# Kernel optimization log

Measured on AMD Instinct MI355X. Metric: run time of the kernel, lower is better.

## Reference

```python
import math
import jax, jax.numpy as jnp
import numpy as np

B, T, C, H = 4, 2048, 1024, 16
HS = C // H


def setup_inputs() -> dict:
    key = jax.random.key(0)
    ks = jax.random.split(key, 5)
    s_in = 1.0 / math.sqrt(C)
    return {
        "x": jax.random.normal(ks[0], (B, T, C), dtype=jnp.float32),
        "w_attn": jax.random.normal(ks[1], (C, 3 * C), dtype=jnp.float32) * s_in,
        "b_attn": jax.random.normal(ks[2], (3 * C,), dtype=jnp.float32) * 0.02,
        "w_proj": jax.random.normal(ks[3], (C, C), dtype=jnp.float32) * s_in,
        "b_proj": jax.random.normal(ks[4], (C,), dtype=jnp.float32) * 0.02,
    }


def reference(x, w_attn, b_attn, w_proj, b_proj):
    Bx, Tx, Cx = x.shape
    hs = Cx // H
    qkv = x @ w_attn + b_attn  # [B, T, 3C]
    q, k, v = jnp.split(qkv, 3, axis=-1)
    # [B, H, T, hs]
    q = q.reshape(Bx, Tx, H, hs).transpose(0, 2, 1, 3)
    k = k.reshape(Bx, Tx, H, hs).transpose(0, 2, 1, 3)
    v = v.reshape(Bx, Tx, H, hs).transpose(0, 2, 1, 3)
    scale = 1.0 / math.sqrt(hs)
    att = jnp.einsum("bhqd,bhkd->bhqk", q, k) * scale  # [B, H, T, T]
    causal = jnp.tril(jnp.ones((Tx, Tx), dtype=bool))
    att = jnp.where(causal, att, -jnp.inf)
    att = jax.nn.softmax(att, axis=-1)
    y = jnp.einsum("bhqk,bhkd->bhqd", att, v)  # [B, H, T, hs]
    y = y.transpose(0, 2, 1, 3).reshape(Bx, Tx, Cx)
    return y @ w_proj + b_proj
```

## Files before the change

### kernel.cpp

```cpp
#include <hip/hip_runtime.h>
#include <stdint.h>

#define Bn 4
#define Tn 2048
#define Cn 1024
#define Hn 16
#define HSn 64
#define Mn (Bn*Tn)
#define N1n (3*Cn)

typedef unsigned short u16;
typedef unsigned int u32;
typedef __attribute__((ext_vector_type(8))) short short8;
typedef __attribute__((ext_vector_type(4))) float f32x4;
typedef __attribute__((ext_vector_type(16))) float f32x16;

__device__ __forceinline__ u16 f2bf(float f){
  u32 u = __float_as_uint(f);
  u += 0x7fffu + ((u >> 16) & 1u);
  return (u16)(u >> 16);
}

__device__ __forceinline__ u32 pkbf(float lo, float hi_){
  u32 r; asm("v_cvt_pk_bf16_f32 %0, %1, %2" : "=v"(r) : "v"(lo), "v"(hi_)); return r;
}

__device__ __forceinline__ float fexp2(float x){
  float r; asm("v_exp_f32 %0, %1" : "=v"(r) : "v"(x)); return r;
}

__device__ __forceinline__ void plswap(u32 &a, u32 &b){
  auto r = __builtin_amdgcn_permlane32_swap(a, b, false, false);
  a = r[0]; b = r[1];
}

__device__ __forceinline__ void gload_lds16(const void* g, void* l){
  __builtin_amdgcn_global_load_lds(
      (const __attribute__((address_space(1))) u32*)g,
      (__attribute__((address_space(3))) u32*)l, 16, 0, 0);
}

#define BARRIER() __builtin_amdgcn_s_barrier()
#define CFENCE() asm volatile("" ::: "memory")

__global__ void k_cvt(const float* __restrict__ in, u16* __restrict__ out, int n8){
  int i = blockIdx.x*256 + threadIdx.x;
  if (i >= n8) return;
  const float4* p = (const float4*)(in) + (size_t)i*2;
  float4 a = p[0], b = p[1];
  uint4 r;
  r.x = (u32)f2bf(a.x) | ((u32)f2bf(a.y) << 16);
  r.y = (u32)f2bf(a.z) | ((u32)f2bf(a.w) << 16);
  r.z = (u32)f2bf(b.x) | ((u32)f2bf(b.y) << 16);
  r.w = (u32)f2bf(b.z) | ((u32)f2bf(b.w) << 16);
  *((uint4*)(out) + i) = r;
}

__global__ void k_tcvt(const float* __restrict__ in, u16* __restrict__ out, int R, int Cc){
  __shared__ float sh[64][68];
  int tid = threadIdx.x;
  int c0 = blockIdx.x*64, r0 = blockIdx.y*64;
  int rr = tid >> 4, c4 = (tid & 15) * 4;
  #pragma unroll
  for (int p=0;p<4;p++){
    int r = rr + 16*p;
    *(float4*)&sh[r][c4] = *(const float4*)&in[(size_t)(r0+r)*Cc + c0 + c4];
  }
  __syncthreads();
  #pragma unroll
  for (int p=0;p<4;p++){
    int oc = rr + 16*p;
    u32 w0 = (u32)f2bf(sh[c4+0][oc]) | ((u32)f2bf(sh[c4+1][oc]) << 16);
    u32 w1 = (u32)f2bf(sh[c4+2][oc]) | ((u32)f2bf(sh[c4+3][oc]) << 16);
    uint2 pk; pk.x = w0; pk.y = w1;
    *(uint2*)&out[(size_t)(c0+oc)*R + r0 + c4] = pk;
  }
}

template <int MODE>
__global__ __launch_bounds__(256, 2)
void k_gemm2(const u16* __restrict__ A, const u16* __restrict__ Bt,
             const float* __restrict__ bias, void* __restrict__ Cout,
             u16* __restrict__ vt, int Nn_, int byPerXcd)
{
  extern __shared__ char smem[];
  const int nkt = 16;
  int tid = threadIdx.x;
  int wave = tid >> 6, lane = tid & 63, g = lane >> 4, cl = lane & 15;
  int wm = wave >> 1, wn = wave & 1;

  int xcd = blockIdx.x & 7, idx = blockIdx.x >> 3;
  int by = xcd * byPerXcd + (idx % byPerXcd);
  int bx = idx / byPerXcd;
  int m0 = by * 128, n0 = bx * 128;

  int srow = tid >> 3;
  int scolb = (tid & 7) << 4;
  int ssw = scolb ^ ((srow & 7) << 4);
  const char* Agp = (const char*)A  + (size_t)(m0 + srow) * 2048 + ssw;
  const char* Bgp = (const char*)Bt + (size_t)(n0 + srow) * 2048 + ssw;

  #define STG(t_, b_) { \
    const char* ag = Agp + (size_t)(t_)*128; \
    const char* bg = Bgp + (size_t)(t_)*128; \
    char* ab = smem + (b_)*32768 + (wave<<10); \
    char* bb = ab + 16384; \
    gload_lds16(ag,          ab); \
    gload_lds16(ag+ 65536,   ab+4096); \
    gload_lds16(ag+131072,   ab+8192); \
    gload_lds16(ag+196608,   ab+12288); \
    gload_lds16(bg,          bb); \
    gload_lds16(bg+ 65536,   bb+4096); \
    gload_lds16(bg+131072,   bb+8192); \
    gload_lds16(bg+196608,   bb+12288); }

  f32x4 acc[4][4];
  #pragma unroll
  for (int i=0;i<4;i++)
    #pragma unroll
    for (int j=0;j<4;j++) acc[i][j] = (f32x4){0.f,0.f,0.f,0.f};

  STG(0, 0);

  for (int t=0; t<nkt; ++t){
    int b = t & 1;
    if (t+1 < nkt){
      STG(t+1, b^1);
      asm volatile("s_waitcnt vmcnt(8)" ::: "memory");
    } else {
      asm volatile("s_waitcnt vmcnt(0)" ::: "memory");
    }
    BARRIER(); CFENCE();
    const char* Asb = smem + b*32768;
    const char* Bsb = Asb + 16384;
    short8 a[4][2], bq[4][2];
    #pragma unroll
    for (int i=0;i<4;i++){
      int row = wm*64 + i*16 + cl;
      #pragma unroll
      for (int ks=0;ks<2;ks++)
        a[i][ks] = *(const short8*)(Asb + row*128 + ((ks*64 + g*16) ^ ((row&7)<<4)));
    }
    #pragma unroll
    for (int j=0;j<4;j++){
      int row = wn*64 + j*16 + cl;
      #pragma unroll
      for (int ks=0;ks<2;ks++)
        bq[j][ks] = *(const short8*)(Bsb + row*128 + ((ks*64 + g*16) ^ ((row&7)<<4)));
    }
    asm volatile("s_waitcnt lgkmcnt(0)" ::: "memory");
    __builtin_amdgcn_s_setprio(1);
    #pragma unroll
    for (int ks=0;ks<2;ks++)
      #pragma unroll
      for (int i=0;i<4;i++)
        #pragma unroll
        for (int j=0;j<4;j++)
          acc[i][j] = __builtin_amdgcn_mfma_f32_16x16x32_bf16(a[i][ks], bq[j][ks], acc[i][j], 0, 0, 0);
    __builtin_amdgcn_s_setprio(0);
    CFENCE(); BARRIER(); CFENCE();
  }
  #undef STG

  #pragma unroll
  for (int jj=0;jj<4;jj++){
    int col = n0 + wn*64 + jj*16 + cl;
    float bj = bias[col];
    if (MODE == 0){
      #pragma unroll
      for (int i=0;i<4;i++){
        int rowb = m0 + wm*64 + i*16 + g*4;
        #pragma unroll
        for (int r=0;r<4;r++)
          ((float*)Cout)[(size_t)(rowb+r)*Nn_ + col] = acc[i][jj][r] + bj;
      }
    } else if (col < 2*Cn){
      #pragma unroll
      for (int i=0;i<4;i++){
        int rowb = m0 + wm*64 + i*16 + g*4;
        #pragma unroll
        for (int r=0;r<4;r++)
          ((u16*)Cout)[(size_t)(rowb+r)*Nn_ + col] = f2bf(acc[i][jj][r] + bj);
      }
    } else {
      int hd = col - 2*Cn;
      #pragma unroll
      for (int i=0;i<4;i++){
        int rowb = m0 + wm*64 + i*16 + g*4;
        int bb = rowb >> 11, tt = rowb & 2047;
        u16* dst = vt + (((size_t)(bb*16 + (hd>>6)))*64 + (hd&63))*2048 + tt;
        uint2 pk;
        pk.x = (u32)f2bf(acc[i][jj][0]+bj) | ((u32)f2bf(acc[i][jj][1]+bj) << 16);
        pk.y = (u32)f2bf(acc[i][jj][2]+bj) | ((u32)f2bf(acc[i][jj][3]+bj) << 16);
        *(uint2*)dst = pk;
      }
    }
  }
}

__global__ __launch_bounds__(256, 4)
void k_attn(const u16* __restrict__ qkv, const u16* __restrict__ vt, u16* __restrict__ yb){
  __shared__ __align__(16) u16 Ks[2][64*64];
  __shared__ __align__(16) u16 Vs[2][64*64];
  int tid = threadIdx.x, wave = tid >> 6, lane = tid & 63;
  int ql = lane & 31, hi = lane >> 5;
  int blk = blockIdx.x;
  int xcd = blk & 7, rest = blk >> 3;
  int bh  = xcd + 8*(rest & 7);
  int qt  = 15 - (rest >> 3);
  int b = bh >> 4, h = bh & 15;

  const u16* Kbase = qkv + (size_t)b*Tn*N1n + Cn + h*HSn;
  const u16* Vbase = vt  + (size_t)bh*HSn*Tn;

  auto STAGE = [&](int bufi, int kt){
    int kb_ = kt*64;
    #pragma unroll
    for (int it=0; it<2; ++it){
      int off = it*4096 + tid*16;
      int row = off >> 7;
      int cb  = off & 127;
      int gc  = (cb ^ ((row & 7) << 4)) >> 1;
      gload_lds16(Kbase + (size_t)(kb_ + row)*N1n + gc,
                  (char*)&Ks[bufi][0] + it*4096 + (wave << 10));
      gload_lds16(Vbase + (size_t)row*Tn + kb_ + gc,
                  (char*)&Vs[bufi][0] + it*4096 + (wave << 10));
    }
  };

  const float QSC = 0.125f * 1.44269504f;

  int q0 = qt * 128;
  int qw0 = q0 + wave*32;
  int qg  = qw0 + ql;
  int ntiles = 2*qt + 2;

  const u16* Qp = qkv + (size_t)(b*Tn + qg)*N1n + h*HSn;
  short8 qf[4];
  #pragma unroll
  for (int dc=0; dc<4; ++dc){
    union { short8 v; u32 w[4]; } qa;
    qa.v = *(const short8*)&Qp[dc*16 + hi*8];
    #pragma unroll
    for (int t=0; t<4; ++t){
      u32 w = qa.w[t];
      float lo = __uint_as_float(w << 16);
      float hf = __uint_as_float(w & 0xffff0000u);
      qa.w[t] = pkbf(lo*QSC, hf*QSC);
    }
    qf[dc] = qa.v;
  }

  f32x16 accO[2];
  #pragma unroll
  for (int f=0; f<2; ++f)
    #pragma unroll
    for (int r=0; r<16; ++r) accO[f][r] = 0.f;
  float m_ = -1e30f, l_ = 0.f;

  STAGE(0, 0);
  asm volatile("s_waitcnt vmcnt(0)" ::: "memory");
  __syncthreads();
  int buf = 0;

  for (int kt=0; kt<ntiles; ++kt){
    if (kt+1 < ntiles) STAGE(buf^1, kt+1);
    const char* Ksb = (const char*)&Ks[buf][0];
    const char* Vsb = (const char*)&Vs[buf][0];
    #pragma unroll
    for (int ksub=0; ksub<2; ++ksub){
      int kbase = kt*64 + ksub*32;
      if (kbase <= qw0 + 31){
        f32x16 s;
        #pragma unroll
        for (int r=0; r<16; ++r) s[r] = 0.f;
        __builtin_amdgcn_s_setprio(1);
        #pragma unroll
        for (int dc=0; dc<4; ++dc){
          short8 kf = *(const short8*)(Ksb + ((ksub*32 + ql) << 7)
                          + ((dc*32 + hi*16) ^ ((ql & 7) << 4)));
          s = __builtin_amdgcn_mfma_f32_32x32x16_bf16(kf, qf[dc], s, 0, 0, 0);
        }
        __builtin_amdgcn_s_setprio(0);
        float p[16];
        if (kbase + 31 > qw0){
          #pragma unroll
          for (int r=0; r<16; ++r){
            int krow = kbase + (r&3) + 8*(r>>2) + 4*hi;
            p[r] = (krow > qg) ? -1e30f : s[r];
          }
        } else {
          #pragma unroll
          for (int r=0; r<16; ++r) p[r] = s[r];
        }
        float t0 = fmaxf(fmaxf(fmaxf(p[0],p[1]),fmaxf(p[2],p[3])),
                         fmaxf(fmaxf(p[4],p[5]),fmaxf(p[6],p[7])));
        float t1 = fmaxf(fmaxf(fmaxf(p[8],p[9]),fmaxf(p[10],p[11])),
                         fmaxf(fmaxf(p[12],p[13]),fmaxf(p[14],p[15])));
        float tm = fmaxf(t0, t1);
        { u32 ua = __float_as_uint(tm), ub = ua; plswap(ua, ub);
          tm = fmaxf(__uint_as_float(ua), __uint_as_float(ub)); }
        if (!__all(tm - m_ <= 8.0f)){
          float mn = fmaxf(m_, tm);
          float al = fexp2(m_ - mn);
          m_ = mn; l_ *= al;
          #pragma unroll
          for (int f=0; f<2; ++f)
            #pragma unroll
            for (int r=0; r<16; ++r) accO[f][r] *= al;
        }
        float ls = 0.f;
        #pragma unroll
        for (int r=0; r<16; ++r){ float e = fexp2(p[r] - m_); p[r] = e; ls += e; }
        { u32 ua = __float_as_uint(ls), ub = ua; plswap(ua, ub);
          l_ += __uint_as_float(ua) + __uint_as_float(ub); }
        #pragma unroll
        for (int ks=0; ks<2; ++ks){
          int pb = ks*8;
          u32 w0 = pkbf(p[pb+0], p[pb+1]);
          u32 w1 = pkbf(p[pb+2], p[pb+3]);
          u32 w2 = pkbf(p[pb+4], p[pb+5]);
          u32 w3 = pkbf(p[pb+6], p[pb+7]);
          plswap(w0, w2);
          plswap(w1, w3);
          union { u32 w[4]; short8 v; } pu;
          pu.w[0] = w0; pu.w[1] = w1; pu.w[2] = w2; pu.w[3] = w3;
          __builtin_amdgcn_s_setprio(1);
          #pragma unroll
          for (int f=0; f<2; ++f){
            short8 vf = *(const short8*)(Vsb + ((f*32 + ql) << 7)
                            + ((ksub*64 + ks*32 + hi*16) ^ ((ql & 7) << 4)));
            accO[f] = __builtin_amdgcn_mfma_f32_32x32x16_bf16(vf, pu.v, accO[f], 0, 0, 0);
          }
          __builtin_amdgcn_s_setprio(0);
        }
      }
    }
    asm volatile("s_waitcnt vmcnt(0)" ::: "memory");
    __syncthreads();
    buf ^= 1;
  }

  float rl = 1.0f / l_;
  u16* yp = yb + (size_t)(b*Tn + qg)*Cn + h*HSn;
  #pragma unroll
  for (int f=0; f<2; ++f)
    #pragma unroll
    for (int rq=0; rq<4; ++rq){
      int d0 = f*32 + rq*8 + hi*4;
      float v0 = accO[f][rq*4+0]*rl, v1 = accO[f][rq*4+1]*rl;
      float v2 = accO[f][rq*4+2]*rl, v3 = accO[f][rq*4+3]*rl;
      uint2 pk2;
      pk2.x = (u32)f2bf(v0) | ((u32)f2bf(v1) << 16);
      pk2.y = (u32)f2bf(v2) | ((u32)f2bf(v3) << 16);
      *(uint2*)&yp[d0] = pk2;
    }
}

extern "C" void kernel_launch(void* const* d_in, const int* in_sizes, int n_in,
                              void* d_out, int out_size, void* d_ws, size_t ws_size,
                              hipStream_t stream)
{
  const float* x      = (const float*)d_in[0];
  const float* w_attn = (const float*)d_in[1];
  const float* b_attn = (const float*)d_in[2];
  const float* w_proj = (const float*)d_in[3];
  const float* b_proj = (const float*)d_in[4];
  float* out = (float*)d_out;
  char* ws = (char*)d_ws;

  size_t off = 0;
  u16* xb  = (u16*)(ws + off); off += (size_t)Mn*Cn*2;
  u16* waT = (u16*)(ws + off); off += (size_t)N1n*Cn*2;
  u16* wpT = (u16*)(ws + off); off += (size_t)Cn*Cn*2;
  u16* qkv = (u16*)(ws + off); off += (size_t)Mn*N1n*2;
  u16* vt  = (u16*)(ws + off); off += (size_t)Bn*Hn*HSn*Tn*2;
  u16* yb  = (u16*)(ws + off); off += (size_t)Mn*Cn*2;

  (void)hipFuncSetAttribute((const void*)k_gemm2<1>,
        hipFuncAttributeMaxDynamicSharedMemorySize, 65536);
  (void)hipFuncSetAttribute((const void*)k_gemm2<0>,
        hipFuncAttributeMaxDynamicSharedMemorySize, 65536);

  k_cvt<<<dim3(Mn*Cn/8/256), 256, 0, stream>>>(x, xb, Mn*Cn/8);
  k_tcvt<<<dim3(N1n/64, Cn/64), 256, 0, stream>>>(w_attn, waT, Cn, N1n);
  k_tcvt<<<dim3(Cn/64, Cn/64), 256, 0, stream>>>(w_proj, wpT, Cn, Cn);
  k_gemm2<1><<<dim3((Mn/128)*(N1n/128)), 256, 65536, stream>>>(xb, waT, b_attn, qkv, vt, N1n, 8);
  k_attn<<<dim3(1024), 256, 0, stream>>>(qkv, vt, yb);
  k_gemm2<0><<<dim3((Mn/128)*(Cn/128)), 256, 65536, stream>>>(yb, wpT, b_proj, out, nullptr, Cn, 8);
}
```

Before: 148.8 us.

## Fuse preprocessing kernels, fold Q scale into GEMM epilogue, reorder attention tiles

Merges the x conversion and both weight transpose-conversions into one launch, removing two kernel launches. Moves the softmax scale for Q into the QKV GEMM epilogue so the attention kernel loads Q fragments directly, without unpacking and rescaling them. Changes the query-tile launch order to interleave long and short causal tiles for better load balance, and uses v_max3 for the row-max reduction. Applying the scale before the bf16 rounding slightly changes numerics.

After: 142.4 us. -4.3%, faster.

```diff
diff --git a/kernel.cpp b/kernel.cpp
--- a/kernel.cpp
+++ b/kernel.cpp
@@ -15,6 +15,8 @@
 typedef __attribute__((ext_vector_type(4))) float f32x4;
 typedef __attribute__((ext_vector_type(16))) float f32x16;
 
+#define QSCf (0.125f * 1.44269504f)
+
 __device__ __forceinline__ u16 f2bf(float f){
   u32 u = __float_as_uint(f);
   u += 0x7fffu + ((u >> 16) & 1u);
@@ -29,6 +31,10 @@
   float r; asm("v_exp_f32 %0, %1" : "=v"(r) : "v"(x)); return r;
 }
 
+__device__ __forceinline__ float fmax3(float a, float b, float c){
+  float r; asm("v_max3_f32 %0, %1, %2, %3" : "=v"(r) : "v"(a), "v"(b), "v"(c)); return r;
+}
+
 __device__ __forceinline__ void plswap(u32 &a, u32 &b){
   auto r = __builtin_amdgcn_permlane32_swap(a, b, false, false);
   a = r[0]; b = r[1];
@@ -43,23 +49,12 @@
 #define BARRIER() __builtin_amdgcn_s_barrier()
 #define CFENCE() asm volatile("" ::: "memory")
 
-__global__ void k_cvt(const float* __restrict__ in, u16* __restrict__ out, int n8){
-  int i = blockIdx.x*256 + threadIdx.x;
-  if (i >= n8) return;
-  const float4* p = (const float4*)(in) + (size_t)i*2;
-  float4 a = p[0], b = p[1];
-  uint4 r;
-  r.x = (u32)f2bf(a.x) | ((u32)f2bf(a.y) << 16);
-  r.y = (u32)f2bf(a.z) | ((u32)f2bf(a.w) << 16);
-  r.z = (u32)f2bf(b.x) | ((u32)f2bf(b.y) << 16);
-  r.w = (u32)f2bf(b.z) | ((u32)f2bf(b.w) << 16);
-  *((uint4*)(out) + i) = r;
-}
-
-__global__ void k_tcvt(const float* __restrict__ in, u16* __restrict__ out, int R, int Cc){
-  __shared__ float sh[64][68];
+__device__ __forceinline__ void tcvt_body(const float* __restrict__ in,
+                                          u16* __restrict__ out,
+                                          int R, int Cc, int bxx, int byy,
+                                          float sh[64][68]){
   int tid = threadIdx.x;
-  int c0 = blockIdx.x*64, r0 = blockIdx.y*64;
+  int c0 = bxx*64, r0 = byy*64;
   int rr = tid >> 4, c4 = (tid & 15) * 4;
   #pragma unroll
   for (int p=0;p<4;p++){
@@ -74,6 +69,31 @@
     u32 w1 = (u32)f2bf(sh[c4+2][oc]) | ((u32)f2bf(sh[c4+3][oc]) << 16);
     uint2 pk; pk.x = w0; pk.y = w1;
     *(uint2*)&out[(size_t)(c0+oc)*R + r0 + c4] = pk;
+  }
+}
+
+__global__ __launch_bounds__(256)
+void k_pre(const float* __restrict__ x, const float* __restrict__ wa,
+           const float* __restrict__ wp, u16* __restrict__ xb,
+           u16* __restrict__ waT, u16* __restrict__ wpT){
+  __shared__ float sh[64][68];
+  int bid = blockIdx.x;
+  if (bid < 4096){
+    int i = bid*256 + threadIdx.x;
+    const float4* p = (const float4*)(x) + (size_t)i*2;
+    float4 a = p[0], b = p[1];
+    uint4 r;
+    r.x = (u32)f2bf(a.x) | ((u32)f2bf(a.y) << 16);
+    r.y = (u32)f2bf(a.z) | ((u32)f2bf(a.w) << 16);
+    r.z = (u32)f2bf(b.x) | ((u32)f2bf(b.y) << 16);
+    r.w = (u32)f2bf(b.z) | ((u32)f2bf(b.w) << 16);
+    *((uint4*)(xb) + i) = r;
+  } else if (bid < 4096 + 768){
+    int b2 = bid - 4096;
+    tcvt_body(wa, waT, Cn, N1n, b2 % 48, b2 / 48, sh);
+  } else {
+    int b3 = bid - 4864;
+    tcvt_body(wp, wpT, Cn, Cn, b3 % 16, b3 / 16, sh);
   }
 }
 
@@ -175,12 +195,13 @@
           ((float*)Cout)[(size_t)(rowb+r)*Nn_ + col] = acc[i][jj][r] + bj;
       }
     } else if (col < 2*Cn){
+      float sc = (col < Cn) ? QSCf : 1.0f;
       #pragma unroll
       for (int i=0;i<4;i++){
         int rowb = m0 + wm*64 + i*16 + g*4;
         #pragma unroll
         for (int r=0;r<4;r++)
-          ((u16*)Cout)[(size_t)(rowb+r)*Nn_ + col] = f2bf(acc[i][jj][r] + bj);
+          ((u16*)Cout)[(size_t)(rowb+r)*Nn_ + col] = f2bf((acc[i][jj][r] + bj) * sc);
       }
     } else {
       int hd = col - 2*Cn;
@@ -207,7 +228,9 @@
   int blk = blockIdx.x;
   int xcd = blk & 7, rest = blk >> 3;
   int bh  = xcd + 8*(rest & 7);
-  int qt  = 15 - (rest >> 3);
+  int qtsel = rest >> 3;
+  int a_ = qtsel & 3, g_ = qtsel >> 2;
+  int qt = (g_==0) ? (15 - a_) : (g_==1) ? (7 - a_) : (g_==2) ? (8 + a_) : a_;
   int b = bh >> 4, h = bh & 15;
 
   const u16* Kbase = qkv + (size_t)b*Tn*N1n + Cn + h*HSn;
@@ -228,8 +251,6 @@
     }
   };
 
-  const float QSC = 0.125f * 1.44269504f;
-
   int q0 = qt * 128;
   int qw0 = q0 + wave*32;
   int qg  = qw0 + ql;
@@ -238,18 +259,7 @@
   const u16* Qp = qkv + (size_t)(b*Tn + qg)*N1n + h*HSn;
   short8 qf[4];
   #pragma unroll
-  for (int dc=0; dc<4; ++dc){
-    union { short8 v; u32 w[4]; } qa;
-    qa.v = *(const short8*)&Qp[dc*16 + hi*8];
-    #pragma unroll
-    for (int t=0; t<4; ++t){
-      u32 w = qa.w[t];
-      float lo = __uint_as_float(w << 16);
-      float hf = __uint_as_float(w & 0xffff0000u);
-      qa.w[t] = pkbf(lo*QSC, hf*QSC);
-    }
-    qf[dc] = qa.v;
-  }
+  for (int dc=0; dc<4; ++dc) qf[dc] = *(const short8*)&Qp[dc*16 + hi*8];
 
   f32x16 accO[2];
   #pragma unroll
@@ -293,11 +303,12 @@
           #pragma unroll
           for (int r=0; r<16; ++r) p[r] = s[r];
         }
-        float t0 = fmaxf(fmaxf(fmaxf(p[0],p[1]),fmaxf(p[2],p[3])),
-                         fmaxf(fmaxf(p[4],p[5]),fmaxf(p[6],p[7])));
-        float t1 = fmaxf(fmaxf(fmaxf(p[8],p[9]),fmaxf(p[10],p[11])),
-                         fmaxf(fmaxf(p[12],p[13]),fmaxf(p[14],p[15])));
-        float tm = fmaxf(t0, t1);
+        float r0 = fmax3(p[0], p[1], p[2]);
+        float r1 = fmax3(p[3], p[4], p[5]);
+        float r2 = fmax3(p[6], p[7], p[8]);
+        float r3 = fmax3(p[9], p[10], p[11]);
+        float r4 = fmax3(p[12], p[13], p[14]);
+        float tm = fmaxf(fmax3(r0, r1, r2), fmax3(r3, r4, p[15]));
         { u32 ua = __float_as_uint(tm), ub = ua; plswap(ua, ub);
           tm = fmaxf(__uint_as_float(ua), __uint_as_float(ub)); }
         if (!__all(tm - m_ <= 8.0f)){
@@ -382,9 +393,7 @@
   (void)hipFuncSetAttribute((const void*)k_gemm2<0>,
         hipFuncAttributeMaxDynamicSharedMemorySize, 65536);
 
-  k_cvt<<<dim3(Mn*Cn/8/256), 256, 0, stream>>>(x, xb, Mn*Cn/8);
-  k_tcvt<<<dim3(N1n/64, Cn/64), 256, 0, stream>>>(w_attn, waT, Cn, N1n);
-  k_tcvt<<<dim3(Cn/64, Cn/64), 256, 0, stream>>>(w_proj, wpT, Cn, Cn);
+  k_pre<<<dim3(5120), 256, 0, stream>>>(x, w_attn, w_proj, xb, waT, wpT);
   k_gemm2<1><<<dim3((Mn/128)*(N1n/128)), 256, 65536, stream>>>(xb, waT, b_attn, qkv, vt, N1n, 8);
   k_attn<<<dim3(1024), 256, 0, stream>>>(qkv, vt, yb);
   k_gemm2<0><<<dim3((Mn/128)*(Cn/128)), 256, 65536, stream>>>(yb, wpT, b_proj, out, nullptr, Cn, 8);
```
